# Kernel optimization log

Hardware: AMD Instinct MI355X
Metric: run time of the kernel (lower is better)

The kernel has to match this reference:

```python
import jax, jax.numpy as jnp
import numpy as np

SCALE, R_MAX, ALPHA = 16, 8, 2.0
HL, WL, C_FEAT = 16, 16, 384
HH, WH = HL * SCALE, WL * SCALE


def bilinear_resize(img, out_h, out_w):
    """PyTorch F.interpolate(mode='bilinear', align_corners=False, antialias=False).
    img: [..., H, W] -> [..., out_h, out_w]."""
    H, W = img.shape[-2], img.shape[-1]
    ys = jnp.maximum((jnp.arange(out_h, dtype=jnp.float32) + 0.5) * (H / out_h) - 0.5, 0.0)
    xs = jnp.maximum((jnp.arange(out_w, dtype=jnp.float32) + 0.5) * (W / out_w) - 0.5, 0.0)
    y0 = jnp.floor(ys).astype(jnp.int32)
    x0 = jnp.floor(xs).astype(jnp.int32)
    y1 = jnp.minimum(y0 + 1, H - 1)
    x1 = jnp.minimum(x0 + 1, W - 1)
    wy = (ys - y0)[:, None]
    wx = (xs - x0)[None, :]
    g = lambda yi, xi: img[..., yi[:, None], xi[None, :]]
    return ((1 - wy) * (1 - wx) * g(y0, x0) + (1 - wy) * wx * g(y0, x1)
            + wy * (1 - wx) * g(y1, x0) + wy * wx * g(y1, x1))


def jbu_forward(feat_lr, guide_hr, sx_raw, sy_raw, th_raw, sr_raw):
    C, Hl, Wl = feat_lr.shape[1], feat_lr.shape[2], feat_lr.shape[3]
    Hh, Wh = guide_hr.shape[2], guide_hr.shape[3]
    scale, R_max, alpha = SCALE, R_MAX, ALPHA
    NEG = -1e30  # finite stand-in for -inf (keeps grads NaN-free)

    # parameter transforms from the module
    sx = jnp.exp(sx_raw[0, 0])
    sy = jnp.exp(sy_raw[0, 0])
    th = jnp.pi * jnp.tanh(th_raw[0, 0])
    sr = jnp.exp(sr_raw[0, 0])

    Y, X = jnp.meshgrid(jnp.arange(Hh, dtype=jnp.float32),
                        jnp.arange(Wh, dtype=jnp.float32), indexing='ij')
    u = (Y + 0.5) / scale - 0.5
    v = (X + 0.5) / scale - 0.5
    uc = jnp.clip(jnp.round(u), 0, Hl - 1).astype(jnp.int32)
    vc = jnp.clip(jnp.round(v), 0, Wl - 1).astype(jnp.int32)

    sigma_eff_hr = bilinear_resize(jnp.maximum(sx, sy), Hh, Wh)
    R_map = jnp.clip(jnp.ceil(alpha * sigma_eff_hr), 1.0, float(R_max))  # [Hh,Wh]

    offs = jnp.arange(-R_max, R_max + 1, dtype=jnp.int32)
    dYg, dXg = jnp.meshgrid(offs, offs, indexing='ij')
    dY = dYg.reshape(-1)[:, None, None]  # [N,1,1]
    dX = dXg.reshape(-1)[:, None, None]

    Ui = jnp.clip(uc[None] + dY, 0, Hl - 1)  # [N,Hh,Wh]
    Vi = jnp.clip(vc[None] + dX, 0, Wl - 1)
    idx = Ui * Wl + Vi                       # flat LR index per (neighbor, HR pixel)
    gat = lambda mp: mp.reshape(-1)[idx]

    sxg = jnp.maximum(gat(sx), 1e-6)
    syg = jnp.maximum(gat(sy), 1e-6)
    thg = gat(th)
    srg = jnp.maximum(gat(sr), 1e-6)

    dx = X[None] - ((Vi.astype(jnp.float32) + 0.5) * scale - 0.5)
    dyv = Y[None] - ((Ui.astype(jnp.float32) + 0.5) * scale - 0.5)
    ct, st = jnp.cos(thg), jnp.sin(thg)
    a = dx * ct + dyv * st
    b = -dx * st + dyv * ct

    guide_lr = bilinear_resize(guide_hr[0], Hl, Wl)  # [3,Hl,Wl]
    g_diff2 = sum((guide_hr[0, c][None] - gat(guide_lr[c])) ** 2 for c in range(3))

    log_w = (-a * a / (2 * sxg ** 2 + 1e-8)
             - b * b / (2 * syg ** 2 + 1e-8)
             - g_diff2 / (2.0 * srg ** 2 + 1e-8))  # [N,Hh,Wh]

    mask = (dY * dY + dX * dX).astype(jnp.float32) <= R_map[None] ** 2
    log_w = jnp.where(mask, log_w, NEG)

    # numerically stable softmax over neighbors (== online-softmax result)
    m = log_w.max(axis=0)
    s = jnp.exp(log_w - m[None])  # masked entries underflow to 0
    den = s.sum(axis=0)           # [Hh,Wh]

    # num[c,h,w] = sum_n s[n,h,w] * feat[idx[n,h,w], c]
    # scatter neighbor weights by LR pixel, then one GEMM with the LR features
    N = idx.shape[0]
    idx2 = idx.reshape(N, Hh * Wh)
    cols = jnp.arange(Hh * Wh, dtype=jnp.int32)[None, :]
    acc = jnp.zeros((Hl * Wl, Hh * Wh), jnp.float32).at[idx2, cols].add(s.reshape(N, -1))
    feat_flat = feat_lr[0].reshape(C, Hl * Wl)  # [C, P]
    num = jnp.einsum('cp,pq->cq', feat_flat, acc).reshape(C, Hh, Wh)

    return (num / jnp.maximum(den, 1e-8)[None])[None]  # [1,C,Hh,Wh]


def setup_inputs() -> dict:
    key = jax.random.key(0)
    k1, k2, k3, k4, k5, k6 = jax.random.split(key, 6)
    feat_lr = jax.random.normal(k1, (1, C_FEAT, HL, WL), jnp.float32)
    guide_hr = jax.random.uniform(k2, (1, 3, HH, WH), dtype=jnp.float32)
    log_sigma = float(np.log(16.0))
    log_sigma_r = float(np.log(0.12))
    sx_raw = log_sigma + 0.1 * jax.random.normal(k3, (1, 1, HL, WL), jnp.float32)
    sy_raw = log_sigma + 0.1 * jax.random.normal(k4, (1, 1, HL, WL), jnp.float32)
    th_raw = 0.1 * jax.random.normal(k5, (1, 1, HL, WL), jnp.float32)
    sr_raw = log_sigma_r + 0.1 * jax.random.normal(k6, (1, 1, HL, WL), jnp.float32)
    return {"feat_lr": feat_lr, "guide_hr": guide_hr, "sx_raw": sx_raw,
            "sy_raw": sy_raw, "th_raw": th_raw, "sr_raw": sr_raw}


def reference(feat_lr, guide_hr, sx_raw, sy_raw, th_raw, sr_raw):
    return jbu_forward(feat_lr, guide_hr, sx_raw, sy_raw, th_raw, sr_raw)
```

## Files before the change

### kernel.cpp

```cpp
#include <hip/hip_runtime.h>
#include <math.h>

#define NEG_BIG (-1e30f)

typedef _Float16 half8 __attribute__((ext_vector_type(8)));
typedef float floatx4 __attribute__((ext_vector_type(4)));

__global__ __launch_bounds__(256) void setup_params(
    const float* __restrict__ sx_raw, const float* __restrict__ sy_raw,
    const float* __restrict__ th_raw, const float* __restrict__ sr_raw,
    const float* __restrict__ guide, float* __restrict__ P)
{
    int t = threadIdx.x;
    float sx = expf(sx_raw[t]);
    float sy = expf(sy_raw[t]);
    float th = 3.14159265358979323846f * tanhf(th_raw[t]);
    float sr = expf(sr_raw[t]);
    float sxg = fmaxf(sx, 1e-6f), syg = fmaxf(sy, 1e-6f), srg = fmaxf(sr, 1e-6f);
    P[0*256 + t] = cosf(th);
    P[1*256 + t] = sinf(th);
    P[2*256 + t] = 1.f / (2.f*sxg*sxg + 1e-8f);
    P[3*256 + t] = 1.f / (2.f*syg*syg + 1e-8f);
    P[4*256 + t] = 1.f / (2.f*srg*srg + 1e-8f);
    int i = t >> 4, j = t & 15;
    int y0 = 16*i + 7, x0 = 16*j + 7;
#pragma unroll
    for (int c = 0; c < 3; ++c) {
        const float* g = guide + c*65536;
        P[(5+c)*256 + t] = 0.25f*(g[y0*256 + x0]     + g[y0*256 + x0 + 1] +
                                  g[(y0+1)*256 + x0] + g[(y0+1)*256 + x0 + 1]);
    }
    P[8*256 + t] = fmaxf(sx, sy);
}

__global__ __launch_bounds__(256) void convert_feat(
    const float* __restrict__ feat, _Float16* __restrict__ feat16)
{
    int i = blockIdx.x * 256 + threadIdx.x;
    feat16[i] = (_Float16)feat[i];
}

__global__ __launch_bounds__(256, 4) void jbu_main(
    const float* __restrict__ guide, const _Float16* __restrict__ feat16,
    const float* __restrict__ P, float* __restrict__ out)
{
    __shared__ float sP[9][256];
    __shared__ __align__(16) _Float16 Wb[32][256];
    __shared__ float red[8][32];
    __shared__ float invden[32];

    const int t = threadIdx.x;
#pragma unroll
    for (int g = 0; g < 9; ++g) sP[g][t] = P[g*256 + t];
    __syncthreads();

    const int q   = t & 31;
    const int grp = t >> 5;
    const int Y = blockIdx.y;
    const int X = (blockIdx.x << 5) + q;
    const float Yf = (float)Y, Xf = (float)X;

    float u = (Yf + 0.5f)*0.0625f - 0.5f;
    float v = (Xf + 0.5f)*0.0625f - 0.5f;
    float ysc = fmaxf(u, 0.f), xsc = fmaxf(v, 0.f);
    int y0 = (int)ysc, x0 = (int)xsc;
    int y1 = min(y0 + 1, 15), x1 = min(x0 + 1, 15);
    float wy = ysc - (float)y0, wx = xsc - (float)x0;
    float s00 = sP[8][y0*16 + x0], s01 = sP[8][y0*16 + x1];
    float s10 = sP[8][y1*16 + x0], s11 = sP[8][y1*16 + x1];
    float sig = (1.f - wy)*((1.f - wx)*s00 + wx*s01)
              +        wy *((1.f - wx)*s10 + wx*s11);
    float Rf = fminf(fmaxf(ceilf(2.f*sig), 1.f), 8.f);
    int Ri = (int)Rf;
    int R2i = Ri*Ri;

    const int uc = Y >> 4, vc = X >> 4;
    const float g0 = guide[          (Y << 8) + X];
    const float g1 = guide[ 65536 + ((Y << 8) + X)];
    const float g2 = guide[131072 + ((Y << 8) + X)];

    float lw[32];
    float mloc = NEG_BIG;
    const int pbase = grp << 5;
#pragma unroll
    for (int pi = 0; pi < 32; ++pi) {
        int p = pbase + pi;
        int Pu = p >> 4, Pv = p & 15;
        int ylo = (Pu == 0)  ? -8 : (Pu - uc);
        int yhi = (Pu == 15) ?  8 : (Pu - uc);
        ylo = max(ylo, -8); yhi = min(yhi, 8);
        int xlo = (Pv == 0)  ? -8 : (Pv - vc);
        int xhi = (Pv == 15) ?  8 : (Pv - vc);
        xlo = max(xlo, -8); xhi = min(xhi, 8);
        int cnt = 0;
        if (ylo <= yhi && xlo <= xhi) {
            for (int dY = ylo; dY <= yhi; ++dY) {
                int lim = R2i - dY*dY;
                if (lim >= 0) {
                    int r = (int)sqrtf((float)lim);
                    int lo = max(xlo, -r), hi = min(xhi, r);
                    cnt += max(0, hi - lo + 1);
                }
            }
        }
        float w = NEG_BIG;
        if (cnt > 0) {
            float ctp = sP[0][p], stp = sP[1][p];
            float iAp = sP[2][p], iBp = sP[3][p], iCp = sP[4][p];
            float dxv = Xf - (16.f*(float)Pv + 7.5f);
            float dyv = Yf - (16.f*(float)Pu + 7.5f);
            float a = dxv*ctp + dyv*stp;
            float b = dyv*ctp - dxv*stp;
            float d0 = g0 - sP[5][p], d1 = g1 - sP[6][p], d2 = g2 - sP[7][p];
            float gd = d0*d0 + d1*d1 + d2*d2;
            w = -(a*a*iAp + b*b*iBp + gd*iCp) + __logf((float)cnt);
            mloc = fmaxf(mloc, w);
        }
        lw[pi] = w;
    }
    red[grp][q] = mloc;
    __syncthreads();
    float m = red[0][q];
#pragma unroll
    for (int g = 1; g < 8; ++g) m = fmaxf(m, red[g][q]);
    __syncthreads();

    float dloc = 0.f;
#pragma unroll
    for (int pi = 0; pi < 32; ++pi) {
        int p = pbase + pi;
        float s = __expf(lw[pi] - m);
        _Float16 h = (_Float16)s;
        int chunk = ((p >> 3) ^ q) & 31;
        Wb[q][chunk*8 + (p & 7)] = h;
        dloc += (float)h;
    }
    red[grp][q] = dloc;
    __syncthreads();
    float den = 0.f;
#pragma unroll
    for (int g = 0; g < 8; ++g) den += red[g][q];
    if (grp == 0) invden[q] = 1.f / fmaxf(den, 1e-8f);
    __syncthreads();

    const int lane = t & 63;
    const int wv   = t >> 6;
    const int mrow = lane & 15;
    const int quad = lane >> 4;
    const int c0   = wv * 96;

    floatx4 acc[6][2] = {};
    const _Float16* fbase = feat16 + (c0 + mrow)*256 + quad*8;

#pragma unroll
    for (int ks = 0; ks < 8; ++ks) {
        half8 a[6];
#pragma unroll
        for (int mt = 0; mt < 6; ++mt)
            a[mt] = *(const half8*)(fbase + mt*16*256 + ks*32);
        half8 b[2];
#pragma unroll
        for (int nt = 0; nt < 2; ++nt) {
            int pix = nt*16 + mrow;
            int chunk = ((ks*4 + quad) ^ pix) & 31;
            b[nt] = *(const half8*)(&Wb[pix][chunk*8]);
        }
#pragma unroll
        for (int mt = 0; mt < 6; ++mt)
#pragma unroll
            for (int nt = 0; nt < 2; ++nt)
                acc[mt][nt] = __builtin_amdgcn_mfma_f32_16x16x32_f16(
                    a[mt], b[nt], acc[mt][nt], 0, 0, 0);
    }

    const int outbase = (Y << 8) + (blockIdx.x << 5);
#pragma unroll
    for (int nt = 0; nt < 2; ++nt) {
        float idv = invden[nt*16 + mrow];
#pragma unroll
        for (int mt = 0; mt < 6; ++mt) {
            int crow = c0 + mt*16 + quad*4;
            float* o = out + (size_t)crow*65536 + outbase + nt*16 + mrow;
#pragma unroll
            for (int r = 0; r < 4; ++r)
                o[(size_t)r*65536] = acc[mt][nt][r] * idv;
        }
    }
}

extern "C" void kernel_launch(void* const* d_in, const int* in_sizes, int n_in,
                              void* d_out, int out_size, void* d_ws, size_t ws_size,
                              hipStream_t stream)
{
    const float* feat   = (const float*)d_in[0];
    const float* guide  = (const float*)d_in[1];
    const float* sx_raw = (const float*)d_in[2];
    const float* sy_raw = (const float*)d_in[3];
    const float* th_raw = (const float*)d_in[4];
    const float* sr_raw = (const float*)d_in[5];
    float* out = (float*)d_out;

    _Float16* feat16 = (_Float16*)d_ws;
    float*    P      = (float*)((char*)d_ws + 256*1024);

    setup_params<<<1, 256, 0, stream>>>(sx_raw, sy_raw, th_raw, sr_raw, guide, P);
    convert_feat<<<384, 256, 0, stream>>>(feat, feat16);
    jbu_main<<<dim3(8, 256), 256, 0, stream>>>(guide, feat16, P, out);
}
```

Baseline: 189.2 us.

## Precompute per-block log-count table and fold rotation into quadratic form coefficients

Merges the parameter setup and feature conversion kernels into one launch. In the main kernel, the neighbor count for every (LR pixel, radius, column half) is computed once per block into a shared table, replacing the per-pixel nested count loops. The rotated anisotropic Gaussian is rewritten as a quadratic form with precomputed A2/B2/C2 coefficients, and parameters are packed into float4 for vectorized shared loads. This adds 16KB of shared memory and lowers the occupancy hint from 4 to 3 blocks in exchange for far less ALU work per pixel.

Result: faster. 166.9 us (-11.8%).

```diff
diff --git a/kernel.cpp b/kernel.cpp
--- a/kernel.cpp
+++ b/kernel.cpp
@@ -4,61 +4,105 @@
 #define NEG_BIG (-1e30f)
 
 typedef _Float16 half8 __attribute__((ext_vector_type(8)));
+typedef _Float16 half2v __attribute__((ext_vector_type(2)));
 typedef float floatx4 __attribute__((ext_vector_type(4)));
 
-__global__ __launch_bounds__(256) void setup_params(
+__global__ __launch_bounds__(256) void setup_all(
+    const float* __restrict__ feat, const float* __restrict__ guide,
     const float* __restrict__ sx_raw, const float* __restrict__ sy_raw,
     const float* __restrict__ th_raw, const float* __restrict__ sr_raw,
-    const float* __restrict__ guide, float* __restrict__ P)
+    _Float16* __restrict__ feat16, float4* __restrict__ PQ,
+    float4* __restrict__ PG)
 {
-    int t = threadIdx.x;
+    const int b = blockIdx.x, t = threadIdx.x;
+    if (b < 384) {
+        int i = b*256 + t;
+        feat16[i] = (_Float16)feat[i];
+        return;
+    }
     float sx = expf(sx_raw[t]);
     float sy = expf(sy_raw[t]);
     float th = 3.14159265358979323846f * tanhf(th_raw[t]);
     float sr = expf(sr_raw[t]);
     float sxg = fmaxf(sx, 1e-6f), syg = fmaxf(sy, 1e-6f), srg = fmaxf(sr, 1e-6f);
-    P[0*256 + t] = cosf(th);
-    P[1*256 + t] = sinf(th);
-    P[2*256 + t] = 1.f / (2.f*sxg*sxg + 1e-8f);
-    P[3*256 + t] = 1.f / (2.f*syg*syg + 1e-8f);
-    P[4*256 + t] = 1.f / (2.f*srg*srg + 1e-8f);
+    float iA = 1.f / (2.f*sxg*sxg + 1e-8f);
+    float iB = 1.f / (2.f*syg*syg + 1e-8f);
+    float iC = 1.f / (2.f*srg*srg + 1e-8f);
+    float ct = cosf(th), st = sinf(th);
+    float A2 = iA*ct*ct + iB*st*st;
+    float B2 = 2.f*ct*st*(iA - iB);
+    float C2 = iA*st*st + iB*ct*ct;
+    PQ[t] = make_float4(A2, B2, C2, iC);
     int i = t >> 4, j = t & 15;
     int y0 = 16*i + 7, x0 = 16*j + 7;
+    float g[3];
 #pragma unroll
     for (int c = 0; c < 3; ++c) {
-        const float* g = guide + c*65536;
-        P[(5+c)*256 + t] = 0.25f*(g[y0*256 + x0]     + g[y0*256 + x0 + 1] +
-                                  g[(y0+1)*256 + x0] + g[(y0+1)*256 + x0 + 1]);
-    }
-    P[8*256 + t] = fmaxf(sx, sy);
+        const float* gp = guide + c*65536;
+        g[c] = 0.25f*(gp[y0*256 + x0]     + gp[y0*256 + x0 + 1] +
+                      gp[(y0+1)*256 + x0] + gp[(y0+1)*256 + x0 + 1]);
+    }
+    PG[t] = make_float4(g[0], g[1], g[2], fmaxf(sx, sy));
 }
 
-__global__ __launch_bounds__(256) void convert_feat(
-    const float* __restrict__ feat, _Float16* __restrict__ feat16)
+__global__ __launch_bounds__(256, 3) void jbu_main(
+    const float* __restrict__ guide, const _Float16* __restrict__ feat16,
+    const float4* __restrict__ PQ, const float4* __restrict__ PG,
+    float* __restrict__ out)
 {
-    int i = blockIdx.x * 256 + threadIdx.x;
-    feat16[i] = (_Float16)feat[i];
-}
-
-__global__ __launch_bounds__(256, 4) void jbu_main(
-    const float* __restrict__ guide, const _Float16* __restrict__ feat16,
-    const float* __restrict__ P, float* __restrict__ out)
-{
-    __shared__ float sP[9][256];
+    __shared__ float4 sPQ[256];
+    __shared__ float4 sPG[256];
+    __shared__ float  LC[4096];
     __shared__ __align__(16) _Float16 Wb[32][256];
     __shared__ float red[8][32];
     __shared__ float invden[32];
 
     const int t = threadIdx.x;
-#pragma unroll
-    for (int g = 0; g < 9; ++g) sP[g][t] = P[g*256 + t];
-    __syncthreads();
+    sPQ[t] = PQ[t];
+    sPG[t] = PG[t];
 
     const int q   = t & 31;
     const int grp = t >> 5;
-    const int Y = blockIdx.y;
-    const int X = (blockIdx.x << 5) + q;
+    const int Y   = blockIdx.y;
+    const int X0  = blockIdx.x << 5;
+    const int X   = X0 + q;
     const float Yf = (float)Y, Xf = (float)X;
+    const int uc  = Y >> 4;
+    const int vc0 = X0 >> 4;
+
+    {
+        const int Pu  = t >> 4;
+        const int col = t & 15;
+        const int Rt  = (col >> 1) + 1;
+        const int vcb = col & 1;
+        const int vc  = vc0 + vcb;
+        const int R2  = Rt * Rt;
+        int ylo = (Pu == 0)  ? -8 : (Pu - uc);
+        int yhi = (Pu == 15) ?  8 : (Pu - uc);
+        ylo = max(ylo, -8); yhi = min(yhi, 8);
+        int cnt[16];
+#pragma unroll
+        for (int Pv = 0; Pv < 16; ++Pv) cnt[Pv] = 0;
+        for (int dY = ylo; dY <= yhi; ++dY) {
+            int lim = R2 - dY*dY;
+            if (lim >= 0) {
+                int r = (int)sqrtf((float)lim);
+#pragma unroll
+                for (int Pv = 0; Pv < 16; ++Pv) {
+                    int xlo = (Pv == 0)  ? -8 : (Pv - vc);
+                    int xhi = (Pv == 15) ?  8 : (Pv - vc);
+                    xlo = max(xlo, -8); xhi = min(xhi, 8);
+                    int lo = max(xlo, -r), hi = min(xhi, r);
+                    cnt[Pv] += max(0, hi - lo + 1);
+                }
+            }
+        }
+#pragma unroll
+        for (int Pv = 0; Pv < 16; ++Pv)
+            LC[(Pu*16 + Pv)*16 + col] =
+                (cnt[Pv] > 0) ? __logf((float)cnt[Pv]) : NEG_BIG;
+    }
+    __syncthreads();
 
     float u = (Yf + 0.5f)*0.0625f - 0.5f;
     float v = (Xf + 0.5f)*0.0625f - 0.5f;
@@ -66,57 +110,34 @@
     int y0 = (int)ysc, x0 = (int)xsc;
     int y1 = min(y0 + 1, 15), x1 = min(x0 + 1, 15);
     float wy = ysc - (float)y0, wx = xsc - (float)x0;
-    float s00 = sP[8][y0*16 + x0], s01 = sP[8][y0*16 + x1];
-    float s10 = sP[8][y1*16 + x0], s11 = sP[8][y1*16 + x1];
+    float s00 = sPG[y0*16 + x0].w, s01 = sPG[y0*16 + x1].w;
+    float s10 = sPG[y1*16 + x0].w, s11 = sPG[y1*16 + x1].w;
     float sig = (1.f - wy)*((1.f - wx)*s00 + wx*s01)
               +        wy *((1.f - wx)*s10 + wx*s11);
     float Rf = fminf(fmaxf(ceilf(2.f*sig), 1.f), 8.f);
-    int Ri = (int)Rf;
-    int R2i = Ri*Ri;
-
-    const int uc = Y >> 4, vc = X >> 4;
+    const int colq = ((int)Rf - 1)*2 + (q >> 4);
+
     const float g0 = guide[          (Y << 8) + X];
     const float g1 = guide[ 65536 + ((Y << 8) + X)];
     const float g2 = guide[131072 + ((Y << 8) + X)];
 
+    const int pbase = grp << 5;
+    const float dy0 = Yf - (16.f*(float)(grp*2) + 7.5f);
     float lw[32];
     float mloc = NEG_BIG;
-    const int pbase = grp << 5;
 #pragma unroll
     for (int pi = 0; pi < 32; ++pi) {
         int p = pbase + pi;
-        int Pu = p >> 4, Pv = p & 15;
-        int ylo = (Pu == 0)  ? -8 : (Pu - uc);
-        int yhi = (Pu == 15) ?  8 : (Pu - uc);
-        ylo = max(ylo, -8); yhi = min(yhi, 8);
-        int xlo = (Pv == 0)  ? -8 : (Pv - vc);
-        int xhi = (Pv == 15) ?  8 : (Pv - vc);
-        xlo = max(xlo, -8); xhi = min(xhi, 8);
-        int cnt = 0;
-        if (ylo <= yhi && xlo <= xhi) {
-            for (int dY = ylo; dY <= yhi; ++dY) {
-                int lim = R2i - dY*dY;
-                if (lim >= 0) {
-                    int r = (int)sqrtf((float)lim);
-                    int lo = max(xlo, -r), hi = min(xhi, r);
-                    cnt += max(0, hi - lo + 1);
-                }
-            }
-        }
-        float w = NEG_BIG;
-        if (cnt > 0) {
-            float ctp = sP[0][p], stp = sP[1][p];
-            float iAp = sP[2][p], iBp = sP[3][p], iCp = sP[4][p];
-            float dxv = Xf - (16.f*(float)Pv + 7.5f);
-            float dyv = Yf - (16.f*(float)Pu + 7.5f);
-            float a = dxv*ctp + dyv*stp;
-            float b = dyv*ctp - dxv*stp;
-            float d0 = g0 - sP[5][p], d1 = g1 - sP[6][p], d2 = g2 - sP[7][p];
-            float gd = d0*d0 + d1*d1 + d2*d2;
-            w = -(a*a*iAp + b*b*iBp + gd*iCp) + __logf((float)cnt);
-            mloc = fmaxf(mloc, w);
-        }
+        float4 Q = sPQ[p];
+        float4 G = sPG[p];
+        float dy = (pi < 16) ? dy0 : (dy0 - 16.f);
+        float dx = Xf - (16.f*(float)(pi & 15) + 7.5f);
+        float d0 = g0 - G.x, d1 = g1 - G.y, d2 = g2 - G.z;
+        float gd = d0*d0 + d1*d1 + d2*d2;
+        float quad = Q.x*(dx*dx) + Q.y*(dx*dy) + Q.z*(dy*dy) + Q.w*gd;
+        float w = LC[p*16 + colq] - quad;
         lw[pi] = w;
+        mloc = fmaxf(mloc, w);
     }
     red[grp][q] = mloc;
     __syncthreads();
@@ -127,13 +148,14 @@
 
     float dloc = 0.f;
 #pragma unroll
-    for (int pi = 0; pi < 32; ++pi) {
+    for (int pi = 0; pi < 32; pi += 2) {
         int p = pbase + pi;
-        float s = __expf(lw[pi] - m);
-        _Float16 h = (_Float16)s;
+        float s0 = __expf(lw[pi]     - m);
+        float s1 = __expf(lw[pi + 1] - m);
+        half2v hh; hh[0] = (_Float16)s0; hh[1] = (_Float16)s1;
         int chunk = ((p >> 3) ^ q) & 31;
-        Wb[q][chunk*8 + (p & 7)] = h;
-        dloc += (float)h;
+        *(half2v*)&Wb[q][chunk*8 + (p & 7)] = hh;
+        dloc += (float)hh[0] + (float)hh[1];
     }
     red[grp][q] = dloc;
     __syncthreads();
@@ -173,7 +195,7 @@
                     a[mt], b[nt], acc[mt][nt], 0, 0, 0);
     }
 
-    const int outbase = (Y << 8) + (blockIdx.x << 5);
+    const int outbase = (Y << 8) + X0;
 #pragma unroll
     for (int nt = 0; nt < 2; ++nt) {
         float idv = invden[nt*16 + mrow];
@@ -201,9 +223,10 @@
     float* out = (float*)d_out;
 
     _Float16* feat16 = (_Float16*)d_ws;
-    float*    P      = (float*)((char*)d_ws + 256*1024);
-
-    setup_params<<<1, 256, 0, stream>>>(sx_raw, sy_raw, th_raw, sr_raw, guide, P);
-    convert_feat<<<384, 256, 0, stream>>>(feat, feat16);
-    jbu_main<<<dim3(8, 256), 256, 0, stream>>>(guide, feat16, P, out);
+    float4*   PQ     = (float4*)((char*)d_ws + 196608);
+    float4*   PG     = (float4*)((char*)d_ws + 196608 + 4096);
+
+    setup_all<<<385, 256, 0, stream>>>(feat, guide, sx_raw, sy_raw, th_raw,
+                                       sr_raw, feat16, PQ, PG);
+    jbu_main<<<dim3(8, 256), 256, 0, stream>>>(guide, feat16, PQ, PG, out);
 }
```
